# Kernel tuning notes

Hardware: AMD Instinct MI355X
Metric: run time of the kernel (lower is better)

## Reference

```python
import jax, jax.numpy as jnp
import numpy as np

B, S, D, H = 2, 2048, 1024, 16
D_H = D // H  # 64


def setup_inputs() -> dict:
    key = jax.random.key(0)
    ks = jax.random.split(key, 12)
    inp = {
        "query": jax.random.normal(ks[0], (B, S, D), dtype=jnp.float32),
        "key":   jax.random.normal(ks[1], (B, S, D), dtype=jnp.float32),
        "value": jax.random.normal(ks[2], (B, S, D), dtype=jnp.float32),
        # causal 0/1 float mask, broadcastable to [B, H, Sq, Sk]; 1 = masked
        "mask":  jnp.broadcast_to(jnp.triu(jnp.ones((S, S), dtype=jnp.float32), k=1)[None, None], (B, 1, S, S)),
    }
    scale = 0.02
    inp["wq"] = jax.random.normal(ks[3], (D, D), dtype=jnp.float32) * scale
    inp["bq"] = jnp.zeros((D,), dtype=jnp.float32)
    inp["wk"] = jax.random.normal(ks[4], (D, D), dtype=jnp.float32) * scale
    inp["bk"] = jnp.zeros((D,), dtype=jnp.float32)
    inp["wv"] = jax.random.normal(ks[5], (D, D), dtype=jnp.float32) * scale
    inp["bv"] = jnp.zeros((D,), dtype=jnp.float32)
    inp["wff"] = jax.random.normal(ks[6], (D, D), dtype=jnp.float32) * scale
    inp["bff"] = jnp.zeros((D,), dtype=jnp.float32)
    return inp


def _split_head(x):
    # [B, S, D] -> [B, H, S, d_h]
    b, s, _ = x.shape
    return x.reshape(b, s, H, D_H).transpose(0, 2, 1, 3)


def reference(query, key, value, mask, wq, bq, wk, bk, wv, bv, wff, bff):
    # QKV projections (torch Linear: x @ W.T + b)
    q = _split_head(query @ wq.T + bq)
    k = _split_head(key @ wk.T + bk)
    v = _split_head(value @ wv.T + bv)
    # scaled dot-product attention
    scores = jnp.einsum("bhqd,bhkd->bhqk", q, k) / jnp.sqrt(jnp.float32(D_H))
    scores = scores + mask * (-1e9)
    attn = jax.nn.softmax(scores, axis=-1)
    out = jnp.einsum("bhqk,bhkd->bhqd", attn, v)
    # concat heads: [B, H, S, d_h] -> [B, S, D]
    out = out.transpose(0, 2, 1, 3).reshape(query.shape[0], query.shape[1], D)
    return out @ wff.T + bff
```

## Files before the change

kernel.cpp:

```cpp
#include <hip/hip_runtime.h>
#include <hip/hip_bf16.h>

#define B_  2
#define S_  2048
#define D_  1024
#define H_  16
#define DH_ 64
#define M_  (B_ * S_)

using bf16x8 = __attribute__((ext_vector_type(8))) short;
using s16x4  = __attribute__((ext_vector_type(4))) short;
using f32x4  = __attribute__((ext_vector_type(4))) float;

__device__ __forceinline__ bf16x8 ldg8(const __hip_bfloat16* p) {
    bf16x8 v;
    __builtin_memcpy(&v, p, 16);
    return v;
}
__device__ __forceinline__ bf16x8 lds8(const void* p) {
    bf16x8 v;
    __builtin_memcpy(&v, p, 16);
    return v;
}
__device__ __forceinline__ f32x4 lds4f(const void* p) {
    f32x4 v;
    __builtin_memcpy(&v, p, 16);
    return v;
}
__device__ __forceinline__ void gll16(const void* g, void* l) {
    __builtin_amdgcn_global_load_lds(
        (const __attribute__((address_space(1))) unsigned int*)g,
        (__attribute__((address_space(3))) unsigned int*)l,
        16, 0, 0);
}
__device__ __forceinline__ short bf16bits(float x) {
    __hip_bfloat16 hv = __float2bfloat16(x);
    short sv;
    __builtin_memcpy(&sv, &hv, 2);
    return sv;
}
__device__ __forceinline__ unsigned cvtpk(float lo, float hi) {
    unsigned r;
    asm("v_cvt_pk_bf16_f32 %0, %1, %2" : "=v"(r) : "v"(lo), "v"(hi));
    return r;
}

__global__ void cvt_w(const float* __restrict__ wq, const float* __restrict__ wk,
                      const float* __restrict__ wv, const float* __restrict__ wff,
                      __hip_bfloat16* __restrict__ Wq, __hip_bfloat16* __restrict__ Wk,
                      __hip_bfloat16* __restrict__ Wv, __hip_bfloat16* __restrict__ Wf) {
    const size_t e = (size_t)(blockIdx.x * 256 + threadIdx.x) * 8;
    const int i = (int)(e >> 20);
    const size_t off = e & (((size_t)1 << 20) - 1);
    const float* src = (i == 0) ? wq : (i == 1) ? wk : (i == 2) ? wv : wff;
    __hip_bfloat16* dst = (i == 0) ? Wq : (i == 1) ? Wk : (i == 2) ? Wv : Wf;
    float4 a, b;
    __builtin_memcpy(&a, src + off, 16);
    __builtin_memcpy(&b, src + off + 4, 16);
    __hip_bfloat16 h[8];
    h[0] = __float2bfloat16(a.x); h[1] = __float2bfloat16(a.y);
    h[2] = __float2bfloat16(a.z); h[3] = __float2bfloat16(a.w);
    h[4] = __float2bfloat16(b.x); h[5] = __float2bfloat16(b.y);
    h[6] = __float2bfloat16(b.z); h[7] = __float2bfloat16(b.w);
    __builtin_memcpy(dst + off, h, 16);
}

__global__ __launch_bounds__(512)
void gemm_qkv(const float* __restrict__ Xq, const float* __restrict__ Xk,
              const float* __restrict__ Xv, const __hip_bfloat16* __restrict__ Wq,
              const __hip_bfloat16* __restrict__ Wk, const __hip_bfloat16* __restrict__ Wv,
              const float* __restrict__ bq, const float* __restrict__ bk,
              const float* __restrict__ bv,
              __hip_bfloat16* __restrict__ Qp, __hip_bfloat16* __restrict__ Kp,
              __hip_bfloat16* __restrict__ Vt) {
    constexpr int K = D_;
    constexpr int N = D_;
    __shared__ __align__(16) char At[2][128][128];
    __shared__ __hip_bfloat16 Wt[2][128][32];

    const int z = blockIdx.z;
    const float* A          = (z == 0) ? Xq : (z == 1) ? Xk : Xv;
    const __hip_bfloat16* W = (z == 0) ? Wq : (z == 1) ? Wk : Wv;
    const float* bias       = (z == 0) ? bq : (z == 1) ? bk : bv;
    const float osc = (z == 0) ? 0.125f * 1.4426950408889634f : 1.f;

    const int lin  = blockIdx.y * 8 + blockIdx.x;
    const int xcd  = lin & 7;
    const int idx  = lin >> 3;
    const int row0 = (xcd * 4 + (idx & 3)) * 128;
    const int col0 = (idx >> 2) * 128;

    const int tid = threadIdx.x;
    const int w   = tid >> 6;
    const int l   = tid & 63;
    const int lr  = l & 15;
    const int lg  = l >> 4;
    const int wr  = (w >> 1) * 32;
    const int wc  = (w & 1) * 64;

    f32x4 acc[2][4] = {};

    auto STAGE = [&](int buf, int k0) {
#pragma unroll
        for (int r = 0; r < 2; ++r) {
            const int row = r * 64 + w * 8 + (l >> 3);
            const int csw = ((l & 7) ^ (row & 7)) * 4;
            gll16(A + (size_t)(row0 + row) * K + k0 + csw,
                  &At[buf][r * 64 + w * 8][0]);
        }
        {
            const int row = w * 16 + (l >> 2);
            const int csw = ((l & 3) ^ (row & 3)) * 8;
            gll16(W + (size_t)(col0 + row) * K + k0 + csw,
                  &Wt[buf][w * 16][0]);
        }
    };

    STAGE(0, 0);
    int cur = 0;
    for (int k0 = 0; k0 < K; k0 += 32) {
        __syncthreads();
        if (k0 + 32 < K) STAGE(cur ^ 1, k0 + 32);
        bf16x8 af[2], wf[4];
#pragma unroll
        for (int m = 0; m < 2; ++m) {
            const int arow = wr + m * 16 + lr;
            const int c0 = (2 * lg) ^ (arow & 7);
            const int c1 = (2 * lg + 1) ^ (arow & 7);
            f32x4 a0 = lds4f(&At[cur][arow][c0 * 16]);
            f32x4 a1 = lds4f(&At[cur][arow][c1 * 16]);
            unsigned uu[4] = { cvtpk(a0[0], a0[1]), cvtpk(a0[2], a0[3]),
                               cvtpk(a1[0], a1[1]), cvtpk(a1[2], a1[3]) };
            __builtin_memcpy(&af[m], uu, 16);
        }
#pragma unroll
        for (int n = 0; n < 4; ++n) {
            const int wrow = wc + n * 16 + lr;
            wf[n] = lds8(&Wt[cur][wrow][(lg ^ (wrow & 3)) * 8]);
        }
#pragma unroll
        for (int m = 0; m < 2; ++m)
#pragma unroll
            for (int n = 0; n < 4; ++n)
                acc[m][n] = __builtin_amdgcn_mfma_f32_16x16x32_bf16(
                    af[m], wf[n], acc[m][n], 0, 0, 0);
        cur ^= 1;
    }

    float bv4[4];
#pragma unroll
    for (int n = 0; n < 4; ++n) bv4[n] = bias[col0 + wc + n * 16 + lr];

    if (z == 2) {
#pragma unroll
        for (int m = 0; m < 2; ++m) {
            const int row_s = row0 + wr + m * 16 + lg * 4;
            const int bq_ = row_s >> 11, s0 = row_s & (S_ - 1);
#pragma unroll
            for (int n = 0; n < 4; ++n) {
                const int col = col0 + wc + n * 16 + lr;
                const int h = col >> 6, d = col & (DH_ - 1);
                s16x4 pk;
#pragma unroll
                for (int r = 0; r < 4; ++r) pk[r] = bf16bits(acc[m][n][r] + bv4[n]);
                __builtin_memcpy(
                    Vt + ((size_t)((bq_ * H_ + h) * DH_) + d) * S_ + s0, &pk, 8);
            }
        }
    } else {
        __hip_bfloat16* out = (z == 0) ? Qp : Kp;
#pragma unroll
        for (int m = 0; m < 2; ++m)
#pragma unroll
            for (int n = 0; n < 4; ++n)
#pragma unroll
                for (int r = 0; r < 4; ++r) {
                    const int row = row0 + wr + m * 16 + lg * 4 + r;
                    const int col = col0 + wc + n * 16 + lr;
                    out[(size_t)row * N + col] =
                        __float2bfloat16((acc[m][n][r] + bv4[n]) * osc);
                }
    }
}

__global__ __launch_bounds__(256)
void gemm_ff(const __hip_bfloat16* __restrict__ A, const __hip_bfloat16* __restrict__ W,
             const float* __restrict__ bias, float* __restrict__ out) {
    constexpr int K = D_;
    constexpr int N = D_;
    __shared__ __hip_bfloat16 At[2][64][32];
    __shared__ __hip_bfloat16 Wt[2][128][32];

    const int lin  = blockIdx.y * 8 + blockIdx.x;
    const int xcd  = lin & 7;
    const int idx  = lin >> 3;
    const int row0 = (xcd * 8 + (idx & 7)) * 64;
    const int col0 = (idx >> 3) * 128;

    const int tid = threadIdx.x;
    const int w   = tid >> 6;
    const int l   = tid & 63;
    const int lr  = l & 15;
    const int lg  = l >> 4;
    const int wr  = (w >> 1) * 32;
    const int wc  = (w & 1) * 64;

    const int srow   = l >> 2;
    const int schunk = l & 3;

    f32x4 acc[2][4] = {};

    auto STAGE = [&](int buf, int k0) {
        {
            const int row = w * 16 + srow;
            const int csw = (schunk ^ (row & 3)) * 8;
            gll16(A + (size_t)(row0 + row) * K + k0 + csw, &At[buf][w * 16][0]);
        }
#pragma unroll
        for (int r = 0; r < 2; ++r) {
            const int row = r * 64 + w * 16 + srow;
            const int csw = (schunk ^ (row & 3)) * 8;
            gll16(W + (size_t)(col0 + row) * K + k0 + csw, &Wt[buf][r * 64 + w * 16][0]);
        }
    };

    STAGE(0, 0);
    int cur = 0;
    for (int k0 = 0; k0 < K; k0 += 32) {
        __syncthreads();
        if (k0 + 32 < K) STAGE(cur ^ 1, k0 + 32);
        bf16x8 af[2], wf[4];
#pragma unroll
        for (int m = 0; m < 2; ++m) {
            const int arow = wr + m * 16 + lr;
            af[m] = lds8(&At[cur][arow][(lg ^ (arow & 3)) * 8]);
        }
#pragma unroll
        for (int n = 0; n < 4; ++n) {
            const int wrow = wc + n * 16 + lr;
            wf[n] = lds8(&Wt[cur][wrow][(lg ^ (wrow & 3)) * 8]);
        }
#pragma unroll
        for (int m = 0; m < 2; ++m)
#pragma unroll
            for (int n = 0; n < 4; ++n)
                acc[m][n] = __builtin_amdgcn_mfma_f32_16x16x32_bf16(
                    af[m], wf[n], acc[m][n], 0, 0, 0);
        cur ^= 1;
    }

    float bv4[4];
#pragma unroll
    for (int n = 0; n < 4; ++n) bv4[n] = bias[col0 + wc + n * 16 + lr];
#pragma unroll
    for (int m = 0; m < 2; ++m)
#pragma unroll
        for (int n = 0; n < 4; ++n)
#pragma unroll
            for (int r = 0; r < 4; ++r) {
                const int row = row0 + wr + m * 16 + lg * 4 + r;
                const int col = col0 + wc + n * 16 + lr;
                out[(size_t)row * N + col] = acc[m][n][r] + bv4[n];
            }
}

__global__ __launch_bounds__(512)
void attn_fwd(const __hip_bfloat16* __restrict__ Qp,
              const __hip_bfloat16* __restrict__ Kp,
              const __hip_bfloat16* __restrict__ Vt,
              __hip_bfloat16* __restrict__ O) {
    __shared__ __hip_bfloat16 Kt[2][64][64];
    __shared__ __hip_bfloat16 Vs[2][64][64];
    __shared__ __hip_bfloat16 Pl[8][16][64];

    const int tid = threadIdx.x;
    const int w   = tid >> 6;
    const int l   = tid & 63;
    const int lr  = l & 15;
    const int lg  = l >> 4;

    const int raw = blockIdx.x;
    const int wg  = (raw & 7) * 64 + (raw >> 3);
    const int xcd = wg >> 6;
    const int loc = wg & 63;
    const int bhi = loc >> 4;
    const int prr = loc & 15;
    const int pr  = (bhi >= 2) ? (15 - prr) : prr;
    const int bh  = xcd * 4 + bhi;
    const int h   = bh & (H_ - 1);
    const int b   = bh >> 4;

    const int sub  = w >> 2;
    const int qb_s = sub ? (31 - pr) : pr;
    const int qw0  = qb_s * 64 + (w & 3) * 16;

    bf16x8 aq[2];
#pragma unroll
    for (int kc = 0; kc < 2; ++kc)
        aq[kc] = ldg8(Qp + (size_t)(b * S_ + qw0 + lr) * D_ + h * DH_ + kc * 32 + lg * 8);

    f32x4 o[4] = {};
    f32x4 rs4 = {};

    const int nkt_max = 32 - pr;

    const int srow   = l >> 3;
    const int schunk = l & 7;
    const int psw    = (lr & 7) << 4;

    auto STAGE = [&](int buf, int kt) {
        const int k0 = kt * 64;
        const int row = w * 8 + srow;
        const int csw = (schunk ^ (row & 7)) * 8;
        gll16(Kp + (size_t)(b * S_ + k0 + row) * D_ + h * DH_ + csw,
              &Kt[buf][w * 8][0]);
        gll16(Vt + ((size_t)((b * H_ + h) * DH_) + row) * S_ + k0 + csw,
              &Vs[buf][w * 8][0]);
    };

    char* prow = (char*)&Pl[w][lr][0];

    auto STEP = [&](int kt, int cur) {
        const int k0 = kt * 64;
        __syncthreads();
        if (kt + 1 < nkt_max) STAGE(cur ^ 1, kt + 1);

        if (kt <= qb_s) {
            f32x4 sc[4] = {};
            __builtin_amdgcn_s_setprio(1);
#pragma unroll
            for (int kk = 0; kk < 4; ++kk) {
                const int krow = kk * 16 + lr;
#pragma unroll
                for (int kc = 0; kc < 2; ++kc) {
                    bf16x8 kf = lds8(&Kt[cur][krow][((kc * 4 + lg) ^ (krow & 7)) * 8]);
                    sc[kk] = __builtin_amdgcn_mfma_f32_16x16x32_bf16(kf, aq[kc], sc[kk], 0, 0, 0);
                }
            }
            __builtin_amdgcn_s_setprio(0);

            const int qrow = qw0 + lr;
            if (kt == qb_s) {
#pragma unroll
                for (int kk = 0; kk < 4; ++kk) {
                    float pv[4];
#pragma unroll
                    for (int r = 0; r < 4; ++r) {
                        const int key = k0 + kk * 16 + lg * 4 + r;
                        pv[r] = (key > qrow) ? 0.f : exp2f(sc[kk][r]);
                        rs4[r] += pv[r];
                    }
                    unsigned uu[2] = { cvtpk(pv[0], pv[1]), cvtpk(pv[2], pv[3]) };
                    __builtin_memcpy(prow + ((kk * 32 + lg * 8) ^ psw), uu, 8);
                }
            } else {
#pragma unroll
                for (int kk = 0; kk < 4; ++kk) {
                    float pv[4];
#pragma unroll
                    for (int r = 0; r < 4; ++r) {
                        pv[r] = exp2f(sc[kk][r]);
                        rs4[r] += pv[r];
                    }
                    unsigned uu[2] = { cvtpk(pv[0], pv[1]), cvtpk(pv[2], pv[3]) };
                    __builtin_memcpy(prow + ((kk * 32 + lg * 8) ^ psw), uu, 8);
                }
            }

            bf16x8 pa[2];
#pragma unroll
            for (int kc = 0; kc < 2; ++kc)
                __builtin_memcpy(&pa[kc], prow + ((kc * 64 + lg * 16) ^ psw), 16);
            __builtin_amdgcn_s_setprio(1);
#pragma unroll
            for (int j = 0; j < 4; ++j) {
                const int vrow = j * 16 + lr;
#pragma unroll
                for (int kc = 0; kc < 2; ++kc) {
                    bf16x8 vf = lds8(&Vs[cur][vrow][((kc * 4 + lg) ^ (vrow & 7)) * 8]);
                    o[j] = __builtin_amdgcn_mfma_f32_16x16x32_bf16(pa[kc], vf, o[j], 0, 0, 0);
                }
            }
            __builtin_amdgcn_s_setprio(0);
        }
    };

    STAGE(0, 0);
    for (int kt = 0; kt < nkt_max; kt += 2) {
        STEP(kt, 0);
        if (kt + 1 < nkt_max) STEP(kt + 1, 1);
    }

    float rsf = rs4[0] + rs4[1] + rs4[2] + rs4[3];
    rsf += __shfl_xor(rsf, 16);
    rsf += __shfl_xor(rsf, 32);
#pragma unroll
    for (int r = 0; r < 4; ++r) {
        const float inv = 1.f / __shfl(rsf, 4 * lg + r);
        const int row = qw0 + 4 * lg + r;
#pragma unroll
        for (int j = 0; j < 4; ++j)
            O[((size_t)(b * S_ + row)) * D_ + h * DH_ + j * 16 + lr] =
                __float2bfloat16(o[j][r] * inv);
    }
}

extern "C" void kernel_launch(void* const* d_in, const int* in_sizes, int n_in,
                              void* d_out, int out_size, void* d_ws, size_t ws_size,
                              hipStream_t stream) {
    const float* q    = (const float*)d_in[0];
    const float* kin  = (const float*)d_in[1];
    const float* vin  = (const float*)d_in[2];
    const float* wq   = (const float*)d_in[4];
    const float* bq   = (const float*)d_in[5];
    const float* wk   = (const float*)d_in[6];
    const float* bk   = (const float*)d_in[7];
    const float* wv   = (const float*)d_in[8];
    const float* bv   = (const float*)d_in[9];
    const float* wff  = (const float*)d_in[10];
    const float* bff  = (const float*)d_in[11];

    char* ws = (char*)d_ws;
    const size_t MB = 1024 * 1024;
    __hip_bfloat16* Wqb = (__hip_bfloat16*)(ws + 24 * MB);
    __hip_bfloat16* Wkb = (__hip_bfloat16*)(ws + 26 * MB);
    __hip_bfloat16* Wvb = (__hip_bfloat16*)(ws + 28 * MB);
    __hip_bfloat16* Wfb = (__hip_bfloat16*)(ws + 30 * MB);
    __hip_bfloat16* Qp  = (__hip_bfloat16*)(ws + 32 * MB);
    __hip_bfloat16* Kp  = (__hip_bfloat16*)(ws + 40 * MB);
    __hip_bfloat16* Vt  = (__hip_bfloat16*)(ws + 48 * MB);
    __hip_bfloat16* Ob  = (__hip_bfloat16*)(ws + 56 * MB);

    cvt_w<<<2048, 256, 0, stream>>>(wq, wk, wv, wff, Wqb, Wkb, Wvb, Wfb);

    dim3 gq(8, 32, 3);
    gemm_qkv<<<gq, 512, 0, stream>>>(q, kin, vin, Wqb, Wkb, Wvb,
                                     bq, bk, bv, Qp, Kp, Vt);

    attn_fwd<<<512, 512, 0, stream>>>(Qp, Kp, Vt, Ob);

    dim3 gg(8, 64);
    gemm_ff<<<gg, 256, 0, stream>>>(Ob, Wfb, bff, (float*)d_out);
}
```

Measured before the change: 131.9 us.

## Deepen GEMM and attention pipelines with multi-stage LDS buffers and software-pipelined QK

The QKV projection GEMM moves from 512 to 256 threads, so each warp computes a 64x64 tile (4x4 MFMA accumulators). It gains a three-stage LDS ring with explicit vmcnt waits in place of __syncthreads double buffering. The attention kernel uses a four-deep K/V ring, prefetches three tiles ahead, and computes the next tile's QK scores before the current tile's softmax and PV, so MFMA work overlaps exp/LDS work. The goal is to hide global-load latency and barrier stalls, at the cost of more LDS and registers and possibly lower occupancy.

```diff
diff --git a/kernel.cpp b/kernel.cpp
--- a/kernel.cpp
+++ b/kernel.cpp
@@ -65,7 +65,7 @@
     __builtin_memcpy(dst + off, h, 16);
 }
 
-__global__ __launch_bounds__(512)
+__global__ __launch_bounds__(256)
 void gemm_qkv(const float* __restrict__ Xq, const float* __restrict__ Xk,
               const float* __restrict__ Xv, const __hip_bfloat16* __restrict__ Wq,
               const __hip_bfloat16* __restrict__ Wk, const __hip_bfloat16* __restrict__ Wv,
@@ -73,10 +73,11 @@
               const float* __restrict__ bv,
               __hip_bfloat16* __restrict__ Qp, __hip_bfloat16* __restrict__ Kp,
               __hip_bfloat16* __restrict__ Vt) {
-    constexpr int K = D_;
-    constexpr int N = D_;
-    __shared__ __align__(16) char At[2][128][128];
-    __shared__ __hip_bfloat16 Wt[2][128][32];
+    constexpr int K  = D_;
+    constexpr int N  = D_;
+    constexpr int NS = K / 32;
+    __shared__ __align__(16) char At[3][128][128];
+    __shared__ __hip_bfloat16 Wt[3][128][32];
 
     const int z = blockIdx.z;
     const float* A          = (z == 0) ? Xq : (z == 1) ? Xk : Xv;
@@ -89,6 +90,131 @@
     const int idx  = lin >> 3;
     const int row0 = (xcd * 4 + (idx & 3)) * 128;
     const int col0 = (idx >> 2) * 128;
+
+    const int tid = threadIdx.x;
+    const int w   = tid >> 6;
+    const int l   = tid & 63;
+    const int lr  = l & 15;
+    const int lg  = l >> 4;
+    const int wr  = (w >> 1) * 64;
+    const int wc  = (w & 1) * 64;
+
+    const int srow4 = l >> 2;
+    const int schk4 = l & 3;
+    const int srow8 = l >> 3;
+    const int schk8 = l & 7;
+
+    f32x4 acc[4][4] = {};
+
+    auto STAGE = [&](int buf, int k0) {
+#pragma unroll
+        for (int r = 0; r < 4; ++r) {
+            const int row = r * 32 + w * 8 + srow8;
+            const int csw = (schk8 ^ (row & 7)) * 4;
+            gll16(A + (size_t)(row0 + row) * K + k0 + csw,
+                  &At[buf][r * 32 + w * 8][0]);
+        }
+#pragma unroll
+        for (int r = 0; r < 2; ++r) {
+            const int row = r * 64 + w * 16 + srow4;
+            const int csw = (schk4 ^ (row & 3)) * 8;
+            gll16(W + (size_t)(col0 + row) * K + k0 + csw,
+                  &Wt[buf][r * 64 + w * 16][0]);
+        }
+    };
+
+    auto COMPUTE = [&](int bc) {
+        bf16x8 af[4], wf[4];
+#pragma unroll
+        for (int m = 0; m < 4; ++m) {
+            const int arow = wr + m * 16 + lr;
+            const int c0 = (2 * lg) ^ (arow & 7);
+            const int c1 = (2 * lg + 1) ^ (arow & 7);
+            f32x4 a0 = lds4f(&At[bc][arow][c0 * 16]);
+            f32x4 a1 = lds4f(&At[bc][arow][c1 * 16]);
+            unsigned uu[4] = { cvtpk(a0[0], a0[1]), cvtpk(a0[2], a0[3]),
+                               cvtpk(a1[0], a1[1]), cvtpk(a1[2], a1[3]) };
+            __builtin_memcpy(&af[m], uu, 16);
+        }
+#pragma unroll
+        for (int n = 0; n < 4; ++n) {
+            const int wrow = wc + n * 16 + lr;
+            wf[n] = lds8(&Wt[bc][wrow][(lg ^ (wrow & 3)) * 8]);
+        }
+#pragma unroll
+        for (int m = 0; m < 4; ++m)
+#pragma unroll
+            for (int n = 0; n < 4; ++n)
+                acc[m][n] = __builtin_amdgcn_mfma_f32_16x16x32_bf16(
+                    af[m], wf[n], acc[m][n], 0, 0, 0);
+    };
+
+    auto ITER = [&](int t, int bc) {
+        if (t + 1 < NS) { asm volatile("s_waitcnt vmcnt(6)" ::: "memory"); }
+        else            { asm volatile("s_waitcnt vmcnt(0)" ::: "memory"); }
+        __builtin_amdgcn_s_barrier();
+        __builtin_amdgcn_sched_barrier(0);
+        if (t + 2 < NS) STAGE((bc + 2) % 3, (t + 2) * 32);
+        COMPUTE(bc);
+    };
+
+    STAGE(0, 0);
+    STAGE(1, 32);
+    for (int t = 0; t < NS; t += 3) {
+        ITER(t, 0);
+        if (t + 1 < NS) ITER(t + 1, 1);
+        if (t + 2 < NS) ITER(t + 2, 2);
+    }
+
+    float bv4[4];
+#pragma unroll
+    for (int n = 0; n < 4; ++n) bv4[n] = bias[col0 + wc + n * 16 + lr];
+
+    if (z == 2) {
+#pragma unroll
+        for (int m = 0; m < 4; ++m) {
+            const int row_s = row0 + wr + m * 16 + lg * 4;
+            const int bq_ = row_s >> 11, s0 = row_s & (S_ - 1);
+#pragma unroll
+            for (int n = 0; n < 4; ++n) {
+                const int col = col0 + wc + n * 16 + lr;
+                const int h = col >> 6, d = col & (DH_ - 1);
+                s16x4 pk;
+#pragma unroll
+                for (int r = 0; r < 4; ++r) pk[r] = bf16bits(acc[m][n][r] + bv4[n]);
+                __builtin_memcpy(
+                    Vt + ((size_t)((bq_ * H_ + h) * DH_) + d) * S_ + s0, &pk, 8);
+            }
+        }
+    } else {
+        __hip_bfloat16* out = (z == 0) ? Qp : Kp;
+#pragma unroll
+        for (int m = 0; m < 4; ++m)
+#pragma unroll
+            for (int n = 0; n < 4; ++n)
+#pragma unroll
+                for (int r = 0; r < 4; ++r) {
+                    const int row = row0 + wr + m * 16 + lg * 4 + r;
+                    const int col = col0 + wc + n * 16 + lr;
+                    out[(size_t)row * N + col] =
+                        __float2bfloat16((acc[m][n][r] + bv4[n]) * osc);
+                }
+    }
+}
+
+__global__ __launch_bounds__(256)
+void gemm_ff(const __hip_bfloat16* __restrict__ A, const __hip_bfloat16* __restrict__ W,
+             const float* __restrict__ bias, float* __restrict__ out) {
+    constexpr int K = D_;
+    constexpr int N = D_;
+    __shared__ __hip_bfloat16 At[2][64][32];
+    __shared__ __hip_bfloat16 Wt[2][128][32];
+
+    const int lin  = blockIdx.y * 8 + blockIdx.x;
+    const int xcd  = lin & 7;
+    const int idx  = lin >> 3;
+    const int row0 = (xcd * 8 + (idx & 7)) * 64;
+    const int col0 = (idx >> 3) * 128;
 
     const int tid = threadIdx.x;
     const int w   = tid >> 6;
@@ -98,21 +224,22 @@
     const int wr  = (w >> 1) * 32;
     const int wc  = (w & 1) * 64;
 
+    const int srow   = l >> 2;
+    const int schunk = l & 3;
+
     f32x4 acc[2][4] = {};
 
     auto STAGE = [&](int buf, int k0) {
+        {
+            const int row = w * 16 + srow;
+            const int csw = (schunk ^ (row & 3)) * 8;
+            gll16(A + (size_t)(row0 + row) * K + k0 + csw, &At[buf][w * 16][0]);
+        }
 #pragma unroll
         for (int r = 0; r < 2; ++r) {
-            const int row = r * 64 + w * 8 + (l >> 3);
-            const int csw = ((l & 7) ^ (row & 7)) * 4;
-            gll16(A + (size_t)(row0 + row) * K + k0 + csw,
-                  &At[buf][r * 64 + w * 8][0]);
-        }
-        {
-            const int row = w * 16 + (l >> 2);
-            const int csw = ((l & 3) ^ (row & 3)) * 8;
-            gll16(W + (size_t)(col0 + row) * K + k0 + csw,
-                  &Wt[buf][w * 16][0]);
+            const int row = r * 64 + w * 16 + srow;
+            const int csw = (schunk ^ (row & 3)) * 8;
+            gll16(W + (size_t)(col0 + row) * K + k0 + csw, &Wt[buf][r * 64 + w * 16][0]);
         }
     };
 
@@ -125,13 +252,7 @@
 #pragma unroll
         for (int m = 0; m < 2; ++m) {
             const int arow = wr + m * 16 + lr;
-            const int c0 = (2 * lg) ^ (arow & 7);
-            const int c1 = (2 * lg + 1) ^ (arow & 7);
-            f32x4 a0 = lds4f(&At[cur][arow][c0 * 16]);
-            f32x4 a1 = lds4f(&At[cur][arow][c1 * 16]);
-            unsigned uu[4] = { cvtpk(a0[0], a0[1]), cvtpk(a0[2], a0[3]),
-                               cvtpk(a1[0], a1[1]), cvtpk(a1[2], a1[3]) };
-            __builtin_memcpy(&af[m], uu, 16);
+            af[m] = lds8(&At[cur][arow][(lg ^ (arow & 3)) * 8]);
         }
 #pragma unroll
         for (int n = 0; n < 4; ++n) {
@@ -150,108 +271,6 @@
     float bv4[4];
 #pragma unroll
     for (int n = 0; n < 4; ++n) bv4[n] = bias[col0 + wc + n * 16 + lr];
-
-    if (z == 2) {
-#pragma unroll
-        for (int m = 0; m < 2; ++m) {
-            const int row_s = row0 + wr + m * 16 + lg * 4;
-            const int bq_ = row_s >> 11, s0 = row_s & (S_ - 1);
-#pragma unroll
-            for (int n = 0; n < 4; ++n) {
-                const int col = col0 + wc + n * 16 + lr;
-                const int h = col >> 6, d = col & (DH_ - 1);
-                s16x4 pk;
-#pragma unroll
-                for (int r = 0; r < 4; ++r) pk[r] = bf16bits(acc[m][n][r] + bv4[n]);
-                __builtin_memcpy(
-                    Vt + ((size_t)((bq_ * H_ + h) * DH_) + d) * S_ + s0, &pk, 8);
-            }
-        }
-    } else {
-        __hip_bfloat16* out = (z == 0) ? Qp : Kp;
-#pragma unroll
-        for (int m = 0; m < 2; ++m)
-#pragma unroll
-            for (int n = 0; n < 4; ++n)
-#pragma unroll
-                for (int r = 0; r < 4; ++r) {
-                    const int row = row0 + wr + m * 16 + lg * 4 + r;
-                    const int col = col0 + wc + n * 16 + lr;
-                    out[(size_t)row * N + col] =
-                        __float2bfloat16((acc[m][n][r] + bv4[n]) * osc);
-                }
-    }
-}
-
-__global__ __launch_bounds__(256)
-void gemm_ff(const __hip_bfloat16* __restrict__ A, const __hip_bfloat16* __restrict__ W,
-             const float* __restrict__ bias, float* __restrict__ out) {
-    constexpr int K = D_;
-    constexpr int N = D_;
-    __shared__ __hip_bfloat16 At[2][64][32];
-    __shared__ __hip_bfloat16 Wt[2][128][32];
-
-    const int lin  = blockIdx.y * 8 + blockIdx.x;
-    const int xcd  = lin & 7;
-    const int idx  = lin >> 3;
-    const int row0 = (xcd * 8 + (idx & 7)) * 64;
-    const int col0 = (idx >> 3) * 128;
-
-    const int tid = threadIdx.x;
-    const int w   = tid >> 6;
-    const int l   = tid & 63;
-    const int lr  = l & 15;
-    const int lg  = l >> 4;
-    const int wr  = (w >> 1) * 32;
-    const int wc  = (w & 1) * 64;
-
-    const int srow   = l >> 2;
-    const int schunk = l & 3;
-
-    f32x4 acc[2][4] = {};
-
-    auto STAGE = [&](int buf, int k0) {
-        {
-            const int row = w * 16 + srow;
-            const int csw = (schunk ^ (row & 3)) * 8;
-            gll16(A + (size_t)(row0 + row) * K + k0 + csw, &At[buf][w * 16][0]);
-        }
-#pragma unroll
-        for (int r = 0; r < 2; ++r) {
-            const int row = r * 64 + w * 16 + srow;
-            const int csw = (schunk ^ (row & 3)) * 8;
-            gll16(W + (size_t)(col0 + row) * K + k0 + csw, &Wt[buf][r * 64 + w * 16][0]);
-        }
-    };
-
-    STAGE(0, 0);
-    int cur = 0;
-    for (int k0 = 0; k0 < K; k0 += 32) {
-        __syncthreads();
-        if (k0 + 32 < K) STAGE(cur ^ 1, k0 + 32);
-        bf16x8 af[2], wf[4];
-#pragma unroll
-        for (int m = 0; m < 2; ++m) {
-            const int arow = wr + m * 16 + lr;
-            af[m] = lds8(&At[cur][arow][(lg ^ (arow & 3)) * 8]);
-        }
-#pragma unroll
-        for (int n = 0; n < 4; ++n) {
-            const int wrow = wc + n * 16 + lr;
-            wf[n] = lds8(&Wt[cur][wrow][(lg ^ (wrow & 3)) * 8]);
-        }
-#pragma unroll
-        for (int m = 0; m < 2; ++m)
-#pragma unroll
-            for (int n = 0; n < 4; ++n)
-                acc[m][n] = __builtin_amdgcn_mfma_f32_16x16x32_bf16(
-                    af[m], wf[n], acc[m][n], 0, 0, 0);
-        cur ^= 1;
-    }
-
-    float bv4[4];
-#pragma unroll
-    for (int n = 0; n < 4; ++n) bv4[n] = bias[col0 + wc + n * 16 + lr];
 #pragma unroll
     for (int m = 0; m < 2; ++m)
 #pragma unroll
@@ -269,8 +288,8 @@
               const __hip_bfloat16* __restrict__ Kp,
               const __hip_bfloat16* __restrict__ Vt,
               __hip_bfloat16* __restrict__ O) {
-    __shared__ __hip_bfloat16 Kt[2][64][64];
-    __shared__ __hip_bfloat16 Vs[2][64][64];
+    __shared__ __hip_bfloat16 Kt[4][64][64];
+    __shared__ __hip_bfloat16 Vs[4][64][64];
     __shared__ __hip_bfloat16 Pl[8][16][64];
 
     const int tid = threadIdx.x;
@@ -302,7 +321,7 @@
     f32x4 o[4] = {};
     f32x4 rs4 = {};
 
-    const int nkt_max = 32 - pr;
+    const int nkt = 32 - pr;
 
     const int srow   = l >> 3;
     const int schunk = l & 7;
@@ -320,75 +339,94 @@
 
     char* prow = (char*)&Pl[w][lr][0];
 
-    auto STEP = [&](int kt, int cur) {
+    auto QK = [&](int buf, f32x4 (&sc)[4]) {
+        __builtin_amdgcn_s_setprio(1);
+#pragma unroll
+        for (int kk = 0; kk < 4; ++kk) {
+            const int krow = kk * 16 + lr;
+#pragma unroll
+            for (int kc = 0; kc < 2; ++kc) {
+                bf16x8 kf = lds8(&Kt[buf][krow][((kc * 4 + lg) ^ (krow & 7)) * 8]);
+                sc[kk] = __builtin_amdgcn_mfma_f32_16x16x32_bf16(kf, aq[kc], sc[kk], 0, 0, 0);
+            }
+        }
+        __builtin_amdgcn_s_setprio(0);
+    };
+
+    auto SMPV = [&](int buf, int kt, f32x4 (&sc)[4]) {
         const int k0 = kt * 64;
-        __syncthreads();
-        if (kt + 1 < nkt_max) STAGE(cur ^ 1, kt + 1);
-
-        if (kt <= qb_s) {
-            f32x4 sc[4] = {};
-            __builtin_amdgcn_s_setprio(1);
+        const int qrow = qw0 + lr;
+        if (kt == qb_s) {
 #pragma unroll
             for (int kk = 0; kk < 4; ++kk) {
-                const int krow = kk * 16 + lr;
-#pragma unroll
-                for (int kc = 0; kc < 2; ++kc) {
-                    bf16x8 kf = lds8(&Kt[cur][krow][((kc * 4 + lg) ^ (krow & 7)) * 8]);
-                    sc[kk] = __builtin_amdgcn_mfma_f32_16x16x32_bf16(kf, aq[kc], sc[kk], 0, 0, 0);
+                float pv[4];
+#pragma unroll
+                for (int r = 0; r < 4; ++r) {
+                    const int key = k0 + kk * 16 + lg * 4 + r;
+                    pv[r] = (key > qrow) ? 0.f : exp2f(sc[kk][r]);
+                    rs4[r] += pv[r];
                 }
-            }
-            __builtin_amdgcn_s_setprio(0);
-
-            const int qrow = qw0 + lr;
-            if (kt == qb_s) {
-#pragma unroll
-                for (int kk = 0; kk < 4; ++kk) {
-                    float pv[4];
-#pragma unroll
-                    for (int r = 0; r < 4; ++r) {
-                        const int key = k0 + kk * 16 + lg * 4 + r;
-                        pv[r] = (key > qrow) ? 0.f : exp2f(sc[kk][r]);
-                        rs4[r] += pv[r];
-                    }
-                    unsigned uu[2] = { cvtpk(pv[0], pv[1]), cvtpk(pv[2], pv[3]) };
-                    __builtin_memcpy(prow + ((kk * 32 + lg * 8) ^ psw), uu, 8);
+                unsigned uu[2] = { cvtpk(pv[0], pv[1]), cvtpk(pv[2], pv[3]) };
+                __builtin_memcpy(prow + ((kk * 32 + lg * 8) ^ psw), uu, 8);
+            }
+        } else {
+#pragma unroll
+            for (int kk = 0; kk < 4; ++kk) {
+                float pv[4];
+#pragma unroll
+                for (int r = 0; r < 4; ++r) {
+                    pv[r] = exp2f(sc[kk][r]);
+                    rs4[r] += pv[r];
                 }
-            } else {
-#pragma unroll
-                for (int kk = 0; kk < 4; ++kk) {
-                    float pv[4];
-#pragma unroll
-                    for (int r = 0; r < 4; ++r) {
-                        pv[r] = exp2f(sc[kk][r]);
-                        rs4[r] += pv[r];
-                    }
-                    unsigned uu[2] = { cvtpk(pv[0], pv[1]), cvtpk(pv[2], pv[3]) };
-                    __builtin_memcpy(prow + ((kk * 32 + lg * 8) ^ psw), uu, 8);
-                }
-            }
-
-            bf16x8 pa[2];
-#pragma unroll
-            for (int kc = 0; kc < 2; ++kc)
-                __builtin_memcpy(&pa[kc], prow + ((kc * 64 + lg * 16) ^ psw), 16);
-            __builtin_amdgcn_s_setprio(1);
-#pragma unroll
-            for (int j = 0; j < 4; ++j) {
-                const int vrow = j * 16 + lr;
-#pragma unroll
-                for (int kc = 0; kc < 2; ++kc) {
-                    bf16x8 vf = lds8(&Vs[cur][vrow][((kc * 4 + lg) ^ (vrow & 7)) * 8]);
-                    o[j] = __builtin_amdgcn_mfma_f32_16x16x32_bf16(pa[kc], vf, o[j], 0, 0, 0);
-                }
-            }
-            __builtin_amdgcn_s_setprio(0);
-        }
-    };
-
-    STAGE(0, 0);
-    for (int kt = 0; kt < nkt_max; kt += 2) {
-        STEP(kt, 0);
-        if (kt + 1 < nkt_max) STEP(kt + 1, 1);
+                unsigned uu[2] = { cvtpk(pv[0], pv[1]), cvtpk(pv[2], pv[3]) };
+                __builtin_memcpy(prow + ((kk * 32 + lg * 8) ^ psw), uu, 8);
+            }
+        }
+
+        bf16x8 pa[2];
+#pragma unroll
+        for (int kc = 0; kc < 2; ++kc)
+            __builtin_memcpy(&pa[kc], prow + ((kc * 64 + lg * 16) ^ psw), 16);
+        __builtin_amdgcn_s_setprio(1);
+#pragma unroll
+        for (int j = 0; j < 4; ++j) {
+            const int vrow = j * 16 + lr;
+#pragma unroll
+            for (int kc = 0; kc < 2; ++kc) {
+                bf16x8 vf = lds8(&Vs[buf][vrow][((kc * 4 + lg) ^ (vrow & 7)) * 8]);
+                o[j] = __builtin_amdgcn_mfma_f32_16x16x32_bf16(pa[kc], vf, o[j], 0, 0, 0);
+            }
+        }
+        __builtin_amdgcn_s_setprio(0);
+    };
+
+    f32x4 scA[4] = {}, scB[4] = {};
+
+    auto ITER = [&](int t, int bc, f32x4 (&scC)[4], f32x4 (&scN)[4]) {
+        if (t + 2 < nkt) { asm volatile("s_waitcnt vmcnt(2)" ::: "memory"); }
+        else             { asm volatile("s_waitcnt vmcnt(0)" ::: "memory"); }
+        __builtin_amdgcn_s_barrier();
+        __builtin_amdgcn_sched_barrier(0);
+        if (t + 3 < nkt) STAGE((bc + 3) & 3, t + 3);
+        if (t + 1 <= qb_s) {
+#pragma unroll
+            for (int i = 0; i < 4; ++i) scN[i] = f32x4{0.f, 0.f, 0.f, 0.f};
+            QK((bc + 1) & 3, scN);
+        }
+        if (t <= qb_s) SMPV(bc, t, scC);
+    };
+
+    STAGE(0, 0); STAGE(1, 1); STAGE(2, 2);
+    asm volatile("s_waitcnt vmcnt(4)" ::: "memory");
+    __builtin_amdgcn_s_barrier();
+    __builtin_amdgcn_sched_barrier(0);
+    QK(0, scA);
+
+    for (int t = 0; t < nkt; t += 4) {
+        ITER(t + 0, 0, scA, scB);
+        if (t + 1 < nkt) ITER(t + 1, 1, scB, scA);
+        if (t + 2 < nkt) ITER(t + 2, 2, scA, scB);
+        if (t + 3 < nkt) ITER(t + 3, 3, scB, scA);
     }
 
     float rsf = rs4[0] + rs4[1] + rs4[2] + rs4[3];
@@ -434,7 +472,7 @@
     cvt_w<<<2048, 256, 0, stream>>>(wq, wk, wv, wff, Wqb, Wkb, Wvb, Wfb);
 
     dim3 gq(8, 32, 3);
-    gemm_qkv<<<gq, 512, 0, stream>>>(q, kin, vin, Wqb, Wkb, Wvb,
+    gemm_qkv<<<gq, 256, 0, stream>>>(q, kin, vin, Wqb, Wkb, Wvb,
                                      bq, bk, bv, Qp, Kp, Vt);
 
     attn_fwd<<<512, 512, 0, stream>>>(Qp, Kp, Vt, Ob);
```

After: 131.6 us. About the same (-0.2%).
